# Kernel optimization log

Hardware: AMD Instinct MI355X
Metric: run time of the kernel (lower is better)

## Reference

```python
import jax, jax.numpy as jnp
import numpy as np

B, S, H = 4, 1024, 2048
NQ, NKV, D = 32, 4, 128
EPS = 1e-6
THETA = 1e6


def setup_inputs() -> dict:
    key = jax.random.key(0)
    k1, k2, k3 = jax.random.split(key, 3)
    hidden = jax.random.normal(k1, (B, S, H), jnp.float32) * 0.02
    w_qkv = jax.random.normal(k2, (H, (NQ + 2 * NKV) * D), jnp.float32) * 0.02
    w_o = jax.random.normal(k3, (NQ * D, H), jnp.float32) * 0.02
    q_norm_w = jnp.ones((D,), jnp.float32)
    k_norm_w = jnp.ones((D,), jnp.float32)
    # rotary tables, broadcast to [B, S, D]
    inv_freq = 1.0 / (THETA ** (jnp.arange(0, D, 2, dtype=jnp.float32) / D))
    freqs = jnp.arange(S, dtype=jnp.float32)[:, None] * inv_freq[None, :]  # [S, D/2]
    emb = jnp.concatenate([freqs, freqs], axis=-1)  # [S, D]
    cos = jnp.broadcast_to(jnp.cos(emb)[None], (B, S, D))
    sin = jnp.broadcast_to(jnp.sin(emb)[None], (B, S, D))
    return {"hidden": hidden, "w_qkv": w_qkv, "w_o": w_o,
            "q_norm_w": q_norm_w, "k_norm_w": k_norm_w, "cos": cos, "sin": sin}


def _rms_norm(x, w):
    xf = x.astype(jnp.float32)
    var = jnp.mean(xf * xf, axis=-1, keepdims=True)
    return (w * (xf * jax.lax.rsqrt(var + EPS))).astype(x.dtype)


def _rotate_half(x):
    h = x.shape[-1] // 2
    return jnp.concatenate([-x[..., h:], x[..., :h]], axis=-1)


def reference(hidden, w_qkv, w_o, q_norm_w, k_norm_w, cos, sin):
    b, s, _ = hidden.shape
    qkv = jnp.einsum('bsh,he->bse', hidden, w_qkv)
    q = qkv[..., : NQ * D].reshape(b, s, NQ, D)
    k = qkv[..., NQ * D: (NQ + NKV) * D].reshape(b, s, NKV, D)
    v = qkv[..., (NQ + NKV) * D:].reshape(b, s, NKV, D)

    # per-head RMSNorm on Q and K
    q = _rms_norm(q, q_norm_w)
    k = _rms_norm(k, k_norm_w)

    # fused RoPE (rotate-half), cos/sin broadcast over heads
    c = cos[:, :, None, :]
    sn = sin[:, :, None, :]
    q = q * c + _rotate_half(q) * sn
    k = k * c + _rotate_half(k) * sn

    # GQA causal flash-attention (prefill, sparse_mode=3 -> causal)
    g = NQ // NKV
    qg = q.reshape(b, s, NKV, g, D)
    scale = 1.0 / jnp.sqrt(jnp.asarray(D, hidden.dtype))
    scores = jnp.einsum('bqkgd,bskd->bkgqs', qg, k) * scale  # [B,NKV,g,S,S]
    causal = jnp.tril(jnp.ones((s, s), bool))
    scores = jnp.where(causal[None, None, None], scores, jnp.finfo(scores.dtype).min)
    probs = jax.nn.softmax(scores, axis=-1)
    out = jnp.einsum('bkgqs,bskd->bqkgd', probs, v).reshape(b, s, NQ * D)
    return jnp.einsum('bse,eh->bsh', out, w_o)
```

## Files before the change

### kernel.cpp

```cpp
#include <hip/hip_runtime.h>

#define BB 4
#define SS 1024
#define HH 2048
#define NQH 32
#define NKVH 4
#define DD 128
#define EQKV 5120

typedef __attribute__((ext_vector_type(8))) short s8v;
typedef __attribute__((ext_vector_type(4))) short s4v;
typedef __attribute__((ext_vector_type(4))) float f4v;

__device__ __forceinline__ unsigned short f2bf(float f) {
  unsigned int u = __builtin_bit_cast(unsigned int, f);
  u += 0x7fffu + ((u >> 16) & 1u);
  return (unsigned short)(u >> 16);
}
__device__ __forceinline__ float bf2f(unsigned short s) {
  unsigned int u = ((unsigned int)s) << 16;
  return __builtin_bit_cast(float, u);
}

__device__ __forceinline__ void async16(unsigned short* lds, const unsigned short* g) {
  __builtin_amdgcn_global_load_lds(
      (const __attribute__((address_space(1))) unsigned int*)g,
      (__attribute__((address_space(3))) unsigned int*)lds, 16, 0, 0);
}


__global__ __launch_bounds__(256) void cvt_bf16(const float* __restrict__ in,
                                                unsigned short* __restrict__ out, int n) {
  int i = (blockIdx.x * 256 + threadIdx.x) * 4;
  if (i >= n) return;
  f4v v = *reinterpret_cast<const f4v*>(in + i);
  s4v o;
#pragma unroll
  for (int j = 0; j < 4; ++j) o[j] = (short)f2bf(v[j]);
  *reinterpret_cast<s4v*>(out + i) = o;
}

__global__ __launch_bounds__(256) void transpose_cvt(const float* __restrict__ in,
                                                     unsigned short* __restrict__ out,
                                                     int K, int N) {
  __shared__ unsigned short T[64][65];
  const int k0 = blockIdx.y * 64, n0 = blockIdx.x * 64;
  const int t = threadIdx.x;
  const int r = t >> 4, c4 = (t & 15) * 4;
#pragma unroll
  for (int i = 0; i < 4; ++i) {
    f4v v = *reinterpret_cast<const f4v*>(&in[(size_t)(k0 + r + i * 16) * N + n0 + c4]);
#pragma unroll
    for (int j = 0; j < 4; ++j) T[r + i * 16][c4 + j] = f2bf(v[j]);
  }
  __syncthreads();
#pragma unroll
  for (int i = 0; i < 4; ++i) {
    int n = r + i * 16;
    s4v o;
#pragma unroll
    for (int j = 0; j < 4; ++j) o[j] = (short)T[c4 + j][n];
    *reinterpret_cast<s4v*>(&out[(size_t)(n0 + n) * K + k0 + c4]) = o;
  }
}

__global__ __launch_bounds__(256) void vtrans(const unsigned short* __restrict__ qkv,
                                              unsigned short* __restrict__ Vt) {
  __shared__ unsigned short T[64][68];
  const int s0 = blockIdx.x * 64;
  const int d0 = blockIdx.y * 64;
  const int bk = blockIdx.z;
  const int b = bk >> 2, hkv = bk & 3;
  const int t = threadIdx.x;
  const int r = t >> 4, c4 = (t & 15) * 4;
  const unsigned short* src = qkv + (size_t)(b * SS + s0) * EQKV + (NQH + NKVH + hkv) * DD + d0;
#pragma unroll
  for (int i = 0; i < 4; ++i) {
    int s = r + i * 16;
    s4v v = *reinterpret_cast<const s4v*>(src + (size_t)s * EQKV + c4);
    *reinterpret_cast<s4v*>(&T[s][c4]) = v;
  }
  __syncthreads();
#pragma unroll
  for (int i = 0; i < 4; ++i) {
    int d = r + i * 16;
    s4v o;
#pragma unroll
    for (int j = 0; j < 4; ++j) o[j] = (short)T[c4 + j][d];
    *reinterpret_cast<s4v*>(&Vt[((size_t)bk * DD + d0 + d) * SS + s0 + c4]) = o;
  }
}

template <bool CF32>
__global__ __launch_bounds__(512) void gemm_256(const unsigned short* __restrict__ A,
                                                const unsigned short* __restrict__ Bt,
                                                void* __restrict__ Cp,
                                                int M, int N, int K, int lda) {
  __shared__ unsigned short RING[4][16384];
  const int tid = threadIdx.x;
  const int ln = tid & 63, w = tid >> 6;
  const int la = ln & 15, quad = ln >> 4;
  const int wr = w >> 2, wc = w & 3;

  const int G = gridDim.x, cpx = G >> 3;
  const int swz = (blockIdx.x & 7) * cpx + (blockIdx.x >> 3);
  const int ytiles = M >> 8;
  const int by = swz % ytiles, bx = swz / ytiles;
  const int m0 = by * 256, n0 = bx * 256;

  f4v acc[8][4] = {};

  const int srow = w * 32 + (ln >> 2);
  const int schunk = (ln & 3) ^ ((ln >> 3) & 3);
  const unsigned short* pA0 = A + (size_t)(m0 + srow) * lda + schunk * 8;
  const unsigned short* pA1 = pA0 + (size_t)16 * lda;
  const unsigned short* pB0 = Bt + (size_t)(n0 + srow) * K + schunk * 8;
  const unsigned short* pB1 = pB0 + (size_t)16 * K;

  const int fch = (quad ^ ((la >> 1) & 3)) * 8;
  const int ar = (wr * 128 + la) * 32;
  const int br = 8192 + (wc * 64 + la) * 32;

#define STAGE(s, koff)                                   \
  async16(&RING[s][w * 1024], pA0 + (koff));             \
  async16(&RING[s][w * 1024 + 512], pA1 + (koff));       \
  async16(&RING[s][8192 + w * 1024], pB0 + (koff));      \
  async16(&RING[s][8192 + w * 1024 + 512], pB1 + (koff));

  STAGE(0, 0)
  STAGE(1, 32)
  STAGE(2, 64)
  asm volatile("s_waitcnt vmcnt(8)" ::: "memory");
  __builtin_amdgcn_s_barrier();

  const int NP = K >> 5;
  const int kend = K - 32;
  int u = 0, ks = 96;
  for (int p = 0; p < NP; ++p) {
    s8v a[8], b[4];
#pragma unroll
    for (int mf = 0; mf < 8; ++mf)
      a[mf] = *reinterpret_cast<const s8v*>(&RING[u][ar + mf * 512 + fch]);
#pragma unroll
    for (int nf = 0; nf < 4; ++nf)
      b[nf] = *reinterpret_cast<const s8v*>(&RING[u][br + nf * 512 + fch]);
    const int s3 = (u + 3) & 3;
    STAGE(s3, ks)
    __builtin_amdgcn_s_setprio(1);
#pragma unroll
    for (int mf = 0; mf < 8; ++mf)
#pragma unroll
      for (int nf = 0; nf < 4; ++nf)
        acc[mf][nf] = __builtin_amdgcn_mfma_f32_16x16x32_bf16(a[mf], b[nf], acc[mf][nf], 0, 0, 0);
    __builtin_amdgcn_s_setprio(0);
    asm volatile("s_waitcnt vmcnt(8)" ::: "memory");
    __builtin_amdgcn_s_barrier();
    u = (u + 1) & 3;
    ks = (ks < kend) ? ks + 32 : ks;
  }
  asm volatile("s_waitcnt vmcnt(0)" ::: "memory");
#undef STAGE

#pragma unroll
  for (int mf = 0; mf < 8; ++mf)
#pragma unroll
    for (int nf = 0; nf < 4; ++nf)
#pragma unroll
      for (int r = 0; r < 4; ++r) {
        int row = m0 + wr * 128 + mf * 16 + quad * 4 + r;
        int col = n0 + wc * 64 + nf * 16 + la;
        if constexpr (CF32) ((float*)Cp)[(size_t)row * N + col] = acc[mf][nf][r];
        else ((unsigned short*)Cp)[(size_t)row * N + col] = f2bf(acc[mf][nf][r]);
      }
}

__global__ __launch_bounds__(256) void attn2(unsigned short* __restrict__ qkv,
                                             const unsigned short* __restrict__ Vt) {
  const int idx = blockIdx.x;
  const int tile = 15 - (idx >> 7);
  const int h = idx & 31;
  const int b = (idx >> 5) & 3;
  const int hkv = h >> 3;
  const int tid = threadIdx.x;
  const int ln = tid & 63, w = tid >> 6;
  const int la = ln & 15, quad = ln >> 4;
  const int qr0 = tile * 64;
  __shared__ unsigned short Ks[64 * 128];
  __shared__ unsigned short Vts[128 * 64];
  __shared__ unsigned short Ps[4][16][64];

  const size_t rowb = (size_t)b * SS;
  s8v qf[4];
  {
    const unsigned short* qrow = qkv + (rowb + qr0 + w * 16 + la) * EQKV + h * DD;
#pragma unroll
    for (int t = 0; t < 4; ++t) qf[t] = *reinterpret_cast<const s8v*>(qrow + t * 32 + quad * 8);
  }
  const unsigned short* kcol = qkv + (NQH + hkv) * DD;
  const unsigned short* vtb = Vt + (size_t)(b * NKVH + hkv) * DD * SS;

  float m_[4], ls[4];
  f4v acc[8] = {};
#pragma unroll
  for (int r = 0; r < 4; ++r) { m_[r] = -1.0e30f; ls[r] = 0.f; }

  const float SC = 0.08838834764831845f;
  const int nkb = tile + 1;
  for (int kb = 0; kb < nkb; ++kb) {
    const int key0 = kb * 64;
    __syncthreads();
#pragma unroll
    for (int i = 0; i < 4; ++i) {
      int row = w * 16 + i * 4 + (ln >> 4);
      int chunk = (ln & 15) ^ (row & 15);
      async16(&Ks[(w * 16 + i * 4) * 128],
              kcol + (rowb + key0 + row) * EQKV + chunk * 8);
    }
#pragma unroll
    for (int i = 0; i < 4; ++i) {
      int row = w * 32 + i * 8 + (ln >> 3);
      int chunk = (ln & 7) ^ (ln >> 3);
      async16(&Vts[(w * 32 + i * 8) * 64],
              vtb + (size_t)row * SS + key0 + chunk * 8);
    }
    __syncthreads();
    f4v sc[4];
#pragma unroll
    for (int kt = 0; kt < 4; ++kt) {
      f4v z = {};
#pragma unroll
      for (int t = 0; t < 4; ++t) {
        s8v kf = *reinterpret_cast<const s8v*>(&Ks[(kt * 16 + la) * 128 + ((t * 4 + quad) ^ la) * 8]);
        z = __builtin_amdgcn_mfma_f32_16x16x32_bf16(qf[t], kf, z, 0, 0, 0);
      }
      sc[kt] = z;
    }
    const bool diag = (kb == nkb - 1);
    float pmax[4];
#pragma unroll
    for (int r = 0; r < 4; ++r) {
      if (diag) {
        int q = qr0 + w * 16 + quad * 4 + r;
#pragma unroll
        for (int kt = 0; kt < 4; ++kt)
          if (key0 + kt * 16 + la > q) sc[kt][r] = -1.0e30f;
      }
      pmax[r] = fmaxf(fmaxf(sc[0][r], sc[1][r]), fmaxf(sc[2][r], sc[3][r]));
    }
    int need = 0;
#pragma unroll
    for (int r = 0; r < 4; ++r) need |= (pmax[r] > m_[r] + 64.0f) ? 1 : 0;
    if (__any(need)) {
#pragma unroll
      for (int r = 0; r < 4; ++r) {
        float mx = pmax[r];
#pragma unroll
        for (int off = 8; off >= 1; off >>= 1) mx = fmaxf(mx, __shfl_xor(mx, off));
        float mnew = fmaxf(m_[r], mx);
        float al = __expf((m_[r] - mnew) * SC);
        m_[r] = mnew;
        ls[r] *= al;
#pragma unroll
        for (int nt = 0; nt < 8; ++nt) acc[nt][r] *= al;
      }
    }
#pragma unroll
    for (int r = 0; r < 4; ++r) {
      const int row = quad * 4 + r;
      const float mS = m_[r] * SC;
#pragma unroll
      for (int kt = 0; kt < 4; ++kt) {
        float p = __expf(__builtin_fmaf(sc[kt][r], SC, -mS));
        ls[r] += p;
        int col = kt * 16 + la;
        Ps[w][row][(((col >> 3) ^ (row & 7)) << 3) | (col & 7)] = f2bf(p);
      }
    }
#pragma unroll
    for (int c = 0; c < 2; ++c) {
      s8v pf = *reinterpret_cast<const s8v*>(&Ps[w][la][(((c * 4 + quad) ^ (la & 7)) << 3)]);
#pragma unroll
      for (int nt = 0; nt < 8; ++nt) {
        s8v vf = *reinterpret_cast<const s8v*>(
            &Vts[(nt * 16 + la) * 64 + ((c * 4 + quad) ^ (la & 7)) * 8]);
        acc[nt] = __builtin_amdgcn_mfma_f32_16x16x32_bf16(pf, vf, acc[nt], 0, 0, 0);
      }
    }
  }
#pragma unroll
  for (int r = 0; r < 4; ++r)
#pragma unroll
    for (int off = 8; off >= 1; off >>= 1) ls[r] += __shfl_xor(ls[r], off);
#pragma unroll
  for (int nt = 0; nt < 8; ++nt)
#pragma unroll
    for (int r = 0; r < 4; ++r) {
      int q = qr0 + w * 16 + quad * 4 + r;
      qkv[(rowb + q) * EQKV + h * DD + nt * 16 + la] = f2bf(acc[nt][r] / ls[r]);
    }
}

template <bool AF32, bool BF32, bool CF32>
__global__ __launch_bounds__(256) void gemm_t(const void* __restrict__ Ap,
                                              const void* __restrict__ Bp,
                                              void* __restrict__ Cp,
                                              int M, int N, int K, int lda) {
  __shared__ unsigned short As[64][40];
  __shared__ unsigned short Bs[64][40];
  const int tid  = threadIdx.x;
  const int lane = tid & 63;
  const int wave = tid >> 6;
  const int la   = lane & 15;
  const int quad = lane >> 4;
  const int m0 = blockIdx.y * 64;
  const int n0 = blockIdx.x * 64;
  const int wm = (wave >> 1) * 32;
  const int wn = (wave & 1) * 32;
  f4v acc[2][2] = {};
  const int ar = tid >> 2, ac = (tid & 3) * 8;
  const int bk = tid >> 3, bn = (tid & 7) * 8;
  for (int k0 = 0; k0 < K; k0 += 32) {
    s8v av;
    if constexpr (AF32) {
      const float* a = (const float*)Ap + (size_t)(m0 + ar) * lda + ac + k0;
      f4v v0 = *reinterpret_cast<const f4v*>(a);
      f4v v1 = *reinterpret_cast<const f4v*>(a + 4);
#pragma unroll
      for (int j = 0; j < 4; ++j) { av[j] = (short)f2bf(v0[j]); av[j + 4] = (short)f2bf(v1[j]); }
    } else {
      av = *reinterpret_cast<const s8v*>((const unsigned short*)Ap + (size_t)(m0 + ar) * lda + ac + k0);
    }
    unsigned short bvs[8];
    if constexpr (BF32) {
      const float* bp = (const float*)Bp + (size_t)(k0 + bk) * N + n0 + bn;
      f4v v0 = *reinterpret_cast<const f4v*>(bp);
      f4v v1 = *reinterpret_cast<const f4v*>(bp + 4);
#pragma unroll
      for (int j = 0; j < 4; ++j) { bvs[j] = f2bf(v0[j]); bvs[j + 4] = f2bf(v1[j]); }
    } else {
      s8v bv = *reinterpret_cast<const s8v*>((const unsigned short*)Bp + (size_t)(k0 + bk) * N + n0 + bn);
#pragma unroll
      for (int j = 0; j < 8; ++j) bvs[j] = (unsigned short)bv[j];
    }
    *reinterpret_cast<s8v*>(&As[ar][ac]) = av;
#pragma unroll
    for (int j = 0; j < 8; ++j) Bs[bn + j][bk] = bvs[j];
    __syncthreads();
#pragma unroll
    for (int mi = 0; mi < 2; ++mi) {
      s8v af = *reinterpret_cast<const s8v*>(&As[wm + mi * 16 + la][quad * 8]);
#pragma unroll
      for (int ni = 0; ni < 2; ++ni) {
        s8v bfr = *reinterpret_cast<const s8v*>(&Bs[wn + ni * 16 + la][quad * 8]);
        acc[mi][ni] = __builtin_amdgcn_mfma_f32_16x16x32_bf16(af, bfr, acc[mi][ni], 0, 0, 0);
      }
    }
    __syncthreads();
  }
#pragma unroll
  for (int mi = 0; mi < 2; ++mi)
#pragma unroll
    for (int ni = 0; ni < 2; ++ni)
#pragma unroll
      for (int r = 0; r < 4; ++r) {
        int row = m0 + wm + mi * 16 + quad * 4 + r;
        int col = n0 + wn + ni * 16 + la;
        if constexpr (CF32) ((float*)Cp)[(size_t)row * N + col] = acc[mi][ni][r];
        else ((unsigned short*)Cp)[(size_t)row * N + col] = f2bf(acc[mi][ni][r]);
      }
}

__global__ __launch_bounds__(64) void attn_slow(unsigned short* __restrict__ qkv) {
  const int tile = blockIdx.x;
  const int h = blockIdx.y;
  const int b = blockIdx.z;
  const int hkv = h >> 3;
  const int lane = threadIdx.x;
  const int la = lane & 15;
  const int quad = lane >> 4;
  const int qr0 = tile * 16;
  __shared__ unsigned short P[16][32];
  __shared__ unsigned short V[32][128];
  const size_t base = (size_t)b * SS * EQKV;
  s8v qf[4];
  {
    const unsigned short* qrow = qkv + base + (size_t)(qr0 + la) * EQKV + h * DD;
#pragma unroll
    for (int t = 0; t < 4; ++t)
      qf[t] = *reinterpret_cast<const s8v*>(qrow + t * 32 + quad * 8);
  }
  const unsigned short* kbase = qkv + base + (NQH + hkv) * DD;
  const unsigned short* vbase = qkv + base + (NQH + NKVH + hkv) * DD;
  float m[4], l[4], al[4];
  f4v acc[8] = {};
#pragma unroll
  for (int r = 0; r < 4; ++r) { m[r] = -1.0e30f; l[r] = 0.f; }
  const float scale = 0.08838834764831845f;
  const int nkb = (qr0 + 16 + 31) >> 5;
  for (int kb = 0; kb < nkb; ++kb) {
    const int key0 = kb * 32;
    __syncthreads();
#pragma unroll
    for (int i = 0; i < 8; ++i) {
      int c = i * 64 + lane;
      int row = c >> 4, col = (c & 15) * 8;
      *reinterpret_cast<s8v*>(&V[row][col]) =
          *reinterpret_cast<const s8v*>(vbase + (size_t)(key0 + row) * EQKV + col);
    }
    f4v s0 = {}, s1 = {};
#pragma unroll
    for (int t = 0; t < 4; ++t) {
      s8v k0f = *reinterpret_cast<const s8v*>(kbase + (size_t)(key0 + la) * EQKV + t * 32 + quad * 8);
      s8v k1f = *reinterpret_cast<const s8v*>(kbase + (size_t)(key0 + 16 + la) * EQKV + t * 32 + quad * 8);
      s0 = __builtin_amdgcn_mfma_f32_16x16x32_bf16(qf[t], k0f, s0, 0, 0, 0);
      s1 = __builtin_amdgcn_mfma_f32_16x16x32_bf16(qf[t], k1f, s1, 0, 0, 0);
    }
#pragma unroll
    for (int r = 0; r < 4; ++r) {
      int q = qr0 + quad * 4 + r;
      float v0 = (key0 + la <= q) ? s0[r] * scale : -1.0e30f;
      float v1 = (key0 + 16 + la <= q) ? s1[r] * scale : -1.0e30f;
      float mx = fmaxf(v0, v1);
#pragma unroll
      for (int off = 8; off >= 1; off >>= 1) mx = fmaxf(mx, __shfl_xor(mx, off));
      float mnew = fmaxf(m[r], mx);
      float p0 = __expf(v0 - mnew);
      float p1 = __expf(v1 - mnew);
      al[r] = __expf(m[r] - mnew);
      m[r] = mnew;
      float rsum = p0 + p1;
#pragma unroll
      for (int off = 8; off >= 1; off >>= 1) rsum += __shfl_xor(rsum, off);
      l[r] = l[r] * al[r] + rsum;
      P[quad * 4 + r][la] = f2bf(p0);
      P[quad * 4 + r][la + 16] = f2bf(p1);
    }
#pragma unroll
    for (int nt = 0; nt < 8; ++nt)
#pragma unroll
      for (int r = 0; r < 4; ++r) acc[nt][r] *= al[r];
    __syncthreads();
    s8v pf = *reinterpret_cast<const s8v*>(&P[la][quad * 8]);
#pragma unroll
    for (int nt = 0; nt < 8; ++nt) {
      s8v vf;
#pragma unroll
      for (int j = 0; j < 8; ++j)
        vf[j] = (short)V[quad * 8 + j][nt * 16 + la];
      acc[nt] = __builtin_amdgcn_mfma_f32_16x16x32_bf16(pf, vf, acc[nt], 0, 0, 0);
    }
  }
#pragma unroll
  for (int nt = 0; nt < 8; ++nt)
#pragma unroll
    for (int r = 0; r < 4; ++r) {
      int q = qr0 + quad * 4 + r;
      qkv[base + (size_t)q * EQKV + h * DD + nt * 16 + la] = f2bf(acc[nt][r] / l[r]);
    }
}

__global__ __launch_bounds__(256) void norm_rope(unsigned short* __restrict__ qkv,
                                                 const float* __restrict__ qw,
                                                 const float* __restrict__ kw,
                                                 const float* __restrict__ cosp,
                                                 const float* __restrict__ sinp) {
  const int h = blockIdx.x;
  const int bs = blockIdx.y * 4 + (threadIdx.x >> 6);
  const int s = bs & (SS - 1);
  const int lane = threadIdx.x & 63;
  const int d0 = lane * 2;
  unsigned short* p = qkv + (size_t)bs * EQKV + h * DD + d0;
  unsigned int u = *reinterpret_cast<const unsigned int*>(p);
  float x0 = bf2f((unsigned short)(u & 0xffff));
  float x1 = bf2f((unsigned short)(u >> 16));
  float ss = x0 * x0 + x1 * x1;
#pragma unroll
  for (int off = 32; off >= 1; off >>= 1) ss += __shfl_xor(ss, off);
  float rs = rsqrtf(ss * (1.0f / 128.0f) + 1e-6f);
  const float* w = (h < NQH) ? qw : kw;
  float n0 = x0 * rs * w[d0];
  float n1 = x1 * rs * w[d0 + 1];
  float o0 = __shfl_xor(n0, 32);
  float o1 = __shfl_xor(n1, 32);
  float r0 = (lane < 32) ? -o0 : o0;
  float r1 = (lane < 32) ? -o1 : o1;
  float c0 = cosp[(size_t)s * DD + d0], c1 = cosp[(size_t)s * DD + d0 + 1];
  float s0 = sinp[(size_t)s * DD + d0], s1 = sinp[(size_t)s * DD + d0 + 1];
  float y0 = n0 * c0 + r0 * s0;
  float y1 = n1 * c1 + r1 * s1;
  unsigned int outv = (unsigned int)f2bf(y0) | ((unsigned int)f2bf(y1) << 16);
  *reinterpret_cast<unsigned int*>(p) = outv;
}

extern "C" void kernel_launch(void* const* d_in, const int* in_sizes, int n_in,
                              void* d_out, int out_size, void* d_ws, size_t ws_size,
                              hipStream_t stream) {
  const float* hidden = (const float*)d_in[0];
  const float* w_qkv  = (const float*)d_in[1];
  const float* w_o    = (const float*)d_in[2];
  const float* q_w    = (const float*)d_in[3];
  const float* k_w    = (const float*)d_in[4];
  const float* cosp   = (const float*)d_in[5];
  const float* sinp   = (const float*)d_in[6];
  float* out = (float*)d_out;

  const int M = BB * SS;
  const size_t szHid  = (size_t)M * HH;
  const size_t szWqkv = (size_t)HH * EQKV;
  const size_t szWo   = (size_t)(NQH * DD) * HH;
  const size_t szQkv  = (size_t)M * EQKV;
  const size_t need = (szHid + szWqkv + szWo + szQkv) * sizeof(unsigned short);

  if (ws_size >= need) {
    unsigned short* hb16  = (unsigned short*)d_ws;
    unsigned short* wqkvT = hb16 + szHid;
    unsigned short* woT   = wqkvT + szWqkv;
    unsigned short* qkv   = woT + szWo;
    unsigned short* Vt    = hb16;

    cvt_bf16<<<(int)(szHid / 1024), 256, 0, stream>>>(hidden, hb16, (int)szHid);
    transpose_cvt<<<dim3(EQKV / 64, HH / 64), 256, 0, stream>>>(w_qkv, wqkvT, HH, EQKV);
    transpose_cvt<<<dim3(HH / 64, (NQH * DD) / 64), 256, 0, stream>>>(w_o, woT, NQH * DD, HH);

    gemm_256<false><<<(M / 256) * (EQKV / 256), 512, 0, stream>>>(
        hb16, wqkvT, qkv, M, EQKV, HH, HH);
    vtrans<<<dim3(SS / 64, DD / 64, BB * NKVH), 256, 0, stream>>>(qkv, Vt);
    norm_rope<<<dim3(NQH + NKVH, M / 4), 256, 0, stream>>>(qkv, q_w, k_w, cosp, sinp);
    attn2<<<2048, 256, 0, stream>>>(qkv, Vt);
    gemm_256<true><<<(M / 256) * (HH / 256), 512, 0, stream>>>(
        qkv, woT, out, M, HH, NQH * DD, EQKV);
  } else {
    unsigned short* qkvb = (unsigned short*)d_ws;
    for (int b = 0; b < BB; ++b) {
      const float* hb = hidden + (size_t)b * SS * HH;
      float* ob = out + (size_t)b * SS * HH;
      gemm_t<true, true, false><<<dim3(EQKV / 64, SS / 64), 256, 0, stream>>>(
          hb, w_qkv, qkvb, SS, EQKV, HH, HH);
      norm_rope<<<dim3(NQH + NKVH, SS / 4), 256, 0, stream>>>(qkvb, q_w, k_w, cosp, sinp);
      attn_slow<<<dim3(SS / 16, NQH, 1), 64, 0, stream>>>(qkvb);
      gemm_t<false, true, true><<<dim3(HH / 64, SS / 64), 256, 0, stream>>>(
          qkvb, w_o, ob, SS, HH, NQH * DD, EQKV);
    }
  }
}
```

Before: 454.7 us.

## Split GEMM k-step into two half-phases with interleaved loads, barriers, and MFMAs

The GEMM main loop is restructured so each k-step loads B and half of A, issues half of the next-stage async copies, runs the MFMAs for that half, then does the same for the other half. Prefetch depth drops from three stages ahead to two, with extra block barriers and sched_barriers inside each iteration. The goal is to interleave LDS reads, global prefetch, and MFMA work more finely and cut register pressure from holding all eight A fragments. The cost is more barriers per iteration and less latency hiding from the shallower prefetch.

```diff
diff --git a/kernel.cpp b/kernel.cpp
--- a/kernel.cpp
+++ b/kernel.cpp
@@ -121,45 +121,72 @@
   const int ar = (wr * 128 + la) * 32;
   const int br = 8192 + (wc * 64 + la) * 32;
 
-#define STAGE(s, koff)                                   \
+#define STAGE_FULL(s, koff)                              \
   async16(&RING[s][w * 1024], pA0 + (koff));             \
   async16(&RING[s][w * 1024 + 512], pA1 + (koff));       \
   async16(&RING[s][8192 + w * 1024], pB0 + (koff));      \
   async16(&RING[s][8192 + w * 1024 + 512], pB1 + (koff));
-
-  STAGE(0, 0)
-  STAGE(1, 32)
-  STAGE(2, 64)
-  asm volatile("s_waitcnt vmcnt(8)" ::: "memory");
+#define STAGE_H1(s, koff)                                \
+  async16(&RING[s][w * 1024], pA0 + (koff));             \
+  async16(&RING[s][8192 + w * 1024], pB0 + (koff));
+#define STAGE_H2(s, koff)                                \
+  async16(&RING[s][w * 1024 + 512], pA1 + (koff));       \
+  async16(&RING[s][8192 + w * 1024 + 512], pB1 + (koff));
+
+  STAGE_FULL(0, 0)
+  STAGE_FULL(1, 32)
+  asm volatile("s_waitcnt vmcnt(4)" ::: "memory");
   __builtin_amdgcn_s_barrier();
 
   const int NP = K >> 5;
   const int kend = K - 32;
-  int u = 0, ks = 96;
-  for (int p = 0; p < NP; ++p) {
-    s8v a[8], b[4];
-#pragma unroll
-    for (int mf = 0; mf < 8; ++mf)
-      a[mf] = *reinterpret_cast<const s8v*>(&RING[u][ar + mf * 512 + fch]);
+  int u = 0, ks = 64;
+  for (int t = 0; t < NP; ++t) {
+    const int s2 = (u + 2) & 3;
+    s8v b[4], alo[4], ahi[4];
 #pragma unroll
     for (int nf = 0; nf < 4; ++nf)
       b[nf] = *reinterpret_cast<const s8v*>(&RING[u][br + nf * 512 + fch]);
-    const int s3 = (u + 3) & 3;
-    STAGE(s3, ks)
+#pragma unroll
+    for (int mf = 0; mf < 4; ++mf)
+      alo[mf] = *reinterpret_cast<const s8v*>(&RING[u][ar + mf * 512 + fch]);
+    STAGE_H1(s2, ks)
+    asm volatile("" ::: "memory");
+    __builtin_amdgcn_s_barrier();
+    __builtin_amdgcn_sched_barrier(0);
     __builtin_amdgcn_s_setprio(1);
 #pragma unroll
-    for (int mf = 0; mf < 8; ++mf)
+    for (int mf = 0; mf < 4; ++mf)
 #pragma unroll
       for (int nf = 0; nf < 4; ++nf)
-        acc[mf][nf] = __builtin_amdgcn_mfma_f32_16x16x32_bf16(a[mf], b[nf], acc[mf][nf], 0, 0, 0);
+        acc[mf][nf] = __builtin_amdgcn_mfma_f32_16x16x32_bf16(alo[mf], b[nf], acc[mf][nf], 0, 0, 0);
     __builtin_amdgcn_s_setprio(0);
-    asm volatile("s_waitcnt vmcnt(8)" ::: "memory");
+    asm volatile("" ::: "memory");
+    __builtin_amdgcn_s_barrier();
+    __builtin_amdgcn_sched_barrier(0);
+#pragma unroll
+    for (int mf = 0; mf < 4; ++mf)
+      ahi[mf] = *reinterpret_cast<const s8v*>(&RING[u][ar + (mf + 4) * 512 + fch]);
+    STAGE_H2(s2, ks)
+    asm volatile("" ::: "memory");
+    __builtin_amdgcn_s_barrier();
+    __builtin_amdgcn_sched_barrier(0);
+    __builtin_amdgcn_s_setprio(1);
+#pragma unroll
+    for (int mf = 0; mf < 4; ++mf)
+#pragma unroll
+      for (int nf = 0; nf < 4; ++nf)
+        acc[mf + 4][nf] = __builtin_amdgcn_mfma_f32_16x16x32_bf16(ahi[mf], b[nf], acc[mf + 4][nf], 0, 0, 0);
+    __builtin_amdgcn_s_setprio(0);
+    asm volatile("s_waitcnt vmcnt(4)" ::: "memory");
     __builtin_amdgcn_s_barrier();
     u = (u + 1) & 3;
     ks = (ks < kend) ? ks + 32 : ks;
   }
   asm volatile("s_waitcnt vmcnt(0)" ::: "memory");
-#undef STAGE
+#undef STAGE_FULL
+#undef STAGE_H1
+#undef STAGE_H2
 
 #pragma unroll
   for (int mf = 0; mf < 8; ++mf)
```

Result: slower. 464.6 us (+2.2%).
